# Kernel optimization log

Measured on AMD Instinct MI355X. Metric: run time of the kernel, lower is better.

The kernel has to match this reference:

```python
import jax, jax.numpy as jnp
import numpy as np

N_NEURONS = 100000
NNZ = 3200000
N_SENSORY = 5000
BATCH = 16
NUM_LAYERS = 8
THRESHOLD = 0.01
TANH_STEEPNESS = 5.0


def setup_inputs() -> dict:
    key = jax.random.key(0)
    k1, k2, k3, k4 = jax.random.split(key, 4)
    inputs = jax.random.uniform(k1, (BATCH, N_SENSORY, NUM_LAYERS), dtype=jnp.float32)
    # sparse connectome in COO form; small values so activations stay in a sane range
    weight_vals = jax.random.normal(k2, (NNZ,), dtype=jnp.float32) * 0.1
    weight_rows = jax.random.randint(k3, (NNZ,), 0, N_NEURONS, dtype=jnp.int32)
    weight_cols = jax.random.randint(k4, (NNZ,), 0, N_NEURONS, dtype=jnp.int32)
    sensory_indices = jnp.arange(N_SENSORY, dtype=jnp.int32)
    return {
        "inputs": inputs,
        "weight_vals": weight_vals,
        "weight_rows": weight_rows,
        "weight_cols": weight_cols,
        "sensory_indices": sensory_indices,
    }


def _spmm(vals, rows, cols, x):
    # x: (N, B); y[r, b] = sum_{e: rows[e]==r} vals[e] * x[cols[e], b]
    return jax.ops.segment_sum(vals[:, None] * x[cols], rows, num_segments=N_NEURONS)


def _activate(y):
    y = jnp.where(y >= THRESHOLD, y, jnp.zeros_like(y))
    return jnp.tanh(TANH_STEEPNESS * y)


def reference(inputs, weight_vals, weight_rows, weight_cols, sensory_indices):
    B, S, T = inputs.shape  # T == num_layers
    # preprocess sensory input: threshold then clamp to <= 1
    inp = jnp.where(inputs >= THRESHOLD, inputs, jnp.zeros_like(inputs))
    inp = jnp.minimum(inp, jnp.ones_like(inp))
    # state x: (N, B)
    full_input = jnp.zeros((N_NEURONS, B), inputs.dtype).at[sensory_indices].add(inp[:, :, 0].T)
    x = _activate(_spmm(weight_vals, weight_rows, weight_cols, full_input))
    acts = []
    for layer in range(1, T):
        # inject sensory input for this time step and clamp to <= 1
        x = x.at[sensory_indices].add(inp[:, :, layer].T)
        x = jnp.minimum(x, jnp.ones_like(x))
        acts.append(x)
        x = _activate(_spmm(weight_vals, weight_rows, weight_cols, x))
    acts.append(x)  # last layer: no injection
    # (T, N, B) -> (B, N, T), matching torch vmap'd cat along time dim
    return jnp.stack(acts, axis=0).transpose(2, 1, 0)
```

## Files before the change

kernel.cpp:

```cpp
#include <hip/hip_runtime.h>


#define N_NEURONS 100000
#define NNZ_CNT   3200000
#define N_SENSORY 5000
#define BATCH     16
#define T_LAYERS  8
#define THRESH    0.01f
#define STEEP     5.0f

#define NB (N_NEURONS * BATCH)
#define NT (N_NEURONS * T_LAYERS)
#define ST (N_SENSORY * T_LAYERS)

#define FXSCALE   17592186044416.0f
#define FXINV     (1.0 / 17592186044416.0)

#define LBITS   9
#define BROWS   (1 << LBITS)
#define NBUCKET ((N_NEURONS + BROWS - 1) / BROWS)
#define EPB     8192
#define NBLK_A  ((NNZ_CNT + EPB - 1) / EPB)

__device__ __forceinline__ float thresh_clamp_inp(float u) {
    u = (u >= THRESH) ? u : 0.0f;
    return fminf(u, 1.0f);
}
__device__ __forceinline__ float activate(float y) {
    y = (y >= THRESH) ? y : 0.0f;
    return tanhf(STEEP * y);
}


__global__ void k_init(const float* __restrict__ inp, float* __restrict__ state0,
                       int* __restrict__ btotal) {
    int stride = gridDim.x * blockDim.x;
    for (int i = blockIdx.x * blockDim.x + threadIdx.x; i < NB; i += stride) {
        int n = i >> 4, b = i & 15;
        float v = 0.0f;
        if (n < N_SENSORY) v = thresh_clamp_inp(inp[b * ST + n * T_LAYERS + 0]);
        state0[i] = v;
        if (i < NBUCKET) btotal[i] = 0;
    }
}

__global__ void __launch_bounds__(1024) k_bcount(const int* __restrict__ rows,
                                                 int* __restrict__ btotal) {
    __shared__ int cnt[NBUCKET];
    const int e0 = blockIdx.x * EPB;
    for (int i = threadIdx.x; i < NBUCKET; i += 1024) cnt[i] = 0;
    __syncthreads();
    #pragma unroll
    for (int i = 0; i < EPB / 1024; ++i) {
        int e = e0 + i * 1024 + threadIdx.x;
        if (e < NNZ_CNT) atomicAdd(&cnt[rows[e] >> LBITS], 1);
    }
    __syncthreads();
    for (int i = threadIdx.x; i < NBUCKET; i += 1024)
        if (cnt[i]) atomicAdd(&btotal[i], cnt[i]);
}

__global__ void k_bscan(const int* __restrict__ btotal, int* __restrict__ bbase,
                        int* __restrict__ bcur, int* __restrict__ row_ptr) {
    __shared__ int lds[256];
    int tid = threadIdx.x;
    int v = (tid < NBUCKET) ? btotal[tid] : 0;
    lds[tid] = v;
    __syncthreads();
    for (int off = 1; off < 256; off <<= 1) {
        int add = (tid >= off) ? lds[tid - off] : 0;
        __syncthreads();
        lds[tid] += add;
        __syncthreads();
    }
    if (tid < NBUCKET) {
        bbase[tid] = lds[tid] - v;
        bcur[tid]  = lds[tid] - v;
    }
    if (tid == 0) { bbase[NBUCKET] = NNZ_CNT; row_ptr[N_NEURONS] = NNZ_CNT; }
}

__global__ void __launch_bounds__(1024) k_passA(const float* __restrict__ vals,
                                                const int* __restrict__ rows,
                                                const int* __restrict__ cols,
                                                int* bcur,
                                                int2* __restrict__ packed_tmp) {
    __shared__ int cnt[NBUCKET];
    __shared__ int base[NBUCKET];
    const int e0 = blockIdx.x * EPB;
    for (int i = threadIdx.x; i < NBUCKET; i += 1024) cnt[i] = 0;
    __syncthreads();
    #pragma unroll
    for (int i = 0; i < EPB / 1024; ++i) {
        int e = e0 + i * 1024 + threadIdx.x;
        if (e < NNZ_CNT) atomicAdd(&cnt[rows[e] >> LBITS], 1);
    }
    __syncthreads();
    for (int i = threadIdx.x; i < NBUCKET; i += 1024) {
        int c = cnt[i];
        base[i] = (c > 0) ? atomicAdd(&bcur[i], c) : 0;
        cnt[i] = 0;
    }
    __syncthreads();
    #pragma unroll
    for (int i = 0; i < EPB / 1024; ++i) {
        int e = e0 + i * 1024 + threadIdx.x;
        if (e < NNZ_CNT) {
            int r = rows[e];
            int k = r >> LBITS;
            int pos = base[k] + atomicAdd(&cnt[k], 1);
            packed_tmp[pos] = make_int2((cols[e] << LBITS) | (r & (BROWS - 1)),
                                        __float_as_int(vals[e]));
        }
    }
}

__global__ void __launch_bounds__(1024) k_passB(const int* __restrict__ bbase,
                                                const int2* __restrict__ packed_tmp,
                                                int2* __restrict__ packed,
                                                int* __restrict__ row_ptr) {
    __shared__ int cnt[BROWS];
    __shared__ int scn[BROWS];
    const int tid = threadIdx.x;
    const int k  = blockIdx.x;
    const int r0 = k * BROWS;
    const int nr = min(BROWS, N_NEURONS - r0);
    const int P0 = bbase[k], P1 = bbase[k + 1];
    for (int i = tid; i < BROWS; i += 1024) cnt[i] = 0;
    __syncthreads();
    for (int i = P0 + tid; i < P1; i += 1024)
        atomicAdd(&cnt[packed_tmp[i].x & (BROWS - 1)], 1);
    __syncthreads();
    if (tid < BROWS) scn[tid] = cnt[tid];
    __syncthreads();
    for (int off = 1; off < BROWS; off <<= 1) {
        int add = (tid < BROWS && tid >= off) ? scn[tid - off] : 0;
        __syncthreads();
        if (tid < BROWS) scn[tid] += add;
        __syncthreads();
    }
    if (tid < BROWS) {
        int ex = P0 + scn[tid] - cnt[tid];
        if (tid < nr) row_ptr[r0 + tid] = ex;
        scn[tid] = ex;
    }
    __syncthreads();
    for (int i = P0 + tid; i < P1; i += 1024) {
        int2 pe = packed_tmp[i];
        int d = atomicAdd(&scn[pe.x & (BROWS - 1)], 1);
        packed[d] = make_int2(pe.x >> LBITS, pe.y);
    }
}

__global__ void __launch_bounds__(256) k_layer(const int* __restrict__ row_ptr,
                                               const int2* __restrict__ packed,
                                               const float* __restrict__ state_in,
                                               const float* __restrict__ inp,
                                               float* __restrict__ plane_out,
                                               int t) {
    int tid = blockIdx.x * blockDim.x + threadIdx.x;
    int r = tid >> 4, b = tid & 15;
    if (r >= N_NEURONS) return;
    int s = row_ptr[r], e = row_ptr[r + 1];
    long long acc = 0;
    for (int base = s; base < e; base += 16) {
        int idx = base + b;
        int2 pe = (idx < e) ? packed[idx] : make_int2(0, 0);
        #pragma unroll
        for (int j = 0; j < 16; ++j) {
            int   c = __shfl(pe.x, j, 16);
            float v = __int_as_float(__shfl(pe.y, j, 16));
            float xv = state_in[c * BATCH + b];
            acc += (long long)llrintf(v * xv * FXSCALE);
        }
    }
    float y = (float)((double)acc * FXINV);
    float a = activate(y);
    if (t < T_LAYERS - 1) {
        if (r < N_SENSORY) a += thresh_clamp_inp(inp[b * ST + r * T_LAYERS + (t + 1)]);
        a = fminf(a, 1.0f);
    }
    plane_out[r * BATCH + b] = a;
}

__global__ void k_out(const float* __restrict__ planes, float* __restrict__ out) {
    int i = blockIdx.x * blockDim.x + threadIdx.x;
    if (i >= NB) return;
    int n = i >> 4, b = i & 15;
    float4 o0, o1;
    o0.x = planes[0 * NB + i]; o0.y = planes[1 * NB + i];
    o0.z = planes[2 * NB + i]; o0.w = planes[3 * NB + i];
    o1.x = planes[4 * NB + i]; o1.y = planes[5 * NB + i];
    o1.z = planes[6 * NB + i]; o1.w = planes[7 * NB + i];
    float4* dst = (float4*)&out[b * NT + n * T_LAYERS];
    dst[0] = o0; dst[1] = o1;
}

__global__ void k2_init(const float* __restrict__ inp, float* __restrict__ state,
                        long long* __restrict__ acc) {
    int stride = gridDim.x * blockDim.x;
    for (int i = blockIdx.x * blockDim.x + threadIdx.x; i < NB; i += stride) {
        int n = i >> 4, b = i & 15;
        float v = 0.0f;
        if (n < N_SENSORY) v = thresh_clamp_inp(inp[b * ST + n * T_LAYERS + 0]);
        state[i] = v;
        acc[i]   = 0LL;
    }
}
__global__ void __launch_bounds__(256) k2_spmm(const float* __restrict__ vals,
                                               const int* __restrict__ rows,
                                               const int* __restrict__ cols,
                                               const float* __restrict__ state,
                                               long long* acc) {
    int tid = blockIdx.x * blockDim.x + threadIdx.x;
    int b = tid & 15;
    int e = tid >> 4;
    int estride = (gridDim.x * blockDim.x) >> 4;
    for (; e < NNZ_CNT; e += estride) {
        int   c  = cols[e];
        float xv = state[c * BATCH + b];
        float v  = vals[e];
        long long fx = llrintf(v * xv * FXSCALE);
        if (fx != 0LL) {
            int r = rows[e];
            atomicAdd((unsigned long long*)&acc[r * BATCH + b], (unsigned long long)fx);
        }
    }
}
__global__ void k2_act_inject(long long* acc, const float* __restrict__ inp,
                              float* __restrict__ state, float* __restrict__ out, int t) {
    int stride = gridDim.x * blockDim.x;
    for (int i = blockIdx.x * blockDim.x + threadIdx.x; i < NB; i += stride) {
        int n = i >> 4, b = i & 15;
        float y = (float)((double)acc[i] * FXINV);
        acc[i] = 0LL;
        float v = activate(y);
        if (n < N_SENSORY) v += thresh_clamp_inp(inp[b * ST + n * T_LAYERS + (t + 1)]);
        v = fminf(v, 1.0f);
        state[i] = v;
        out[b * NT + n * T_LAYERS + t] = v;
    }
}
__global__ void k2_act_final(const long long* __restrict__ acc, float* __restrict__ out) {
    int stride = gridDim.x * blockDim.x;
    for (int i = blockIdx.x * blockDim.x + threadIdx.x; i < NB; i += stride) {
        int n = i >> 4, b = i & 15;
        float y = (float)((double)acc[i] * FXINV);
        out[b * NT + n * T_LAYERS + (T_LAYERS - 1)] = activate(y);
    }
}

extern "C" void kernel_launch(void* const* d_in, const int* in_sizes, int n_in,
                              void* d_out, int out_size, void* d_ws, size_t ws_size,
                              hipStream_t stream) {
    const float* inputs = (const float*)d_in[0];
    const float* vals   = (const float*)d_in[1];
    const int*   rows   = (const int*)  d_in[2];
    const int*   cols   = (const int*)  d_in[3];
    float* out = (float*)d_out;

    const size_t sz_planes = (size_t)T_LAYERS * NB * 4;
    const size_t sz_packed = (size_t)NNZ_CNT * 8;
    const size_t sz_rowptr = ((size_t)N_NEURONS + 2) * 4;
    const size_t sz_btotal = (size_t)(NBUCKET + 8) * 4;
    const size_t sz_bbase  = (size_t)(NBUCKET + 8) * 4;
    const size_t sz_bcur   = (size_t)(NBUCKET + 8) * 4;
    const size_t REQ = sz_planes + sz_packed + sz_rowptr + sz_btotal + sz_bbase + sz_bcur;

    const int block = 256;

    if (ws_size >= REQ) {
        char* ws = (char*)d_ws;
        float* planes  = (float*)ws;
        int2*  packed  = (int2*)(ws + sz_planes);
        int*   row_ptr = (int*)(ws + sz_planes + sz_packed);
        int*   btotal  = (int*)(ws + sz_planes + sz_packed + sz_rowptr);
        int*   bbase   = (int*)(ws + sz_planes + sz_packed + sz_rowptr + sz_btotal);
        int*   bcur    = (int*)(ws + sz_planes + sz_packed + sz_rowptr + sz_btotal + sz_bbase);
        float* state0  = planes + (size_t)(T_LAYERS - 1) * NB;
        int2*  packed_tmp = (int2*)planes;

        const int grid_nb = (NB + block - 1) / block;

        k_init<<<grid_nb, block, 0, stream>>>(inputs, state0, btotal);
        k_bcount<<<NBLK_A, 1024, 0, stream>>>(rows, btotal);
        k_bscan<<<1, 256, 0, stream>>>(btotal, bbase, bcur, row_ptr);
        k_passA<<<NBLK_A, 1024, 0, stream>>>(vals, rows, cols, bcur, packed_tmp);
        k_passB<<<NBUCKET, 1024, 0, stream>>>(bbase, packed_tmp, packed, row_ptr);

        for (int t = 0; t < T_LAYERS; ++t) {
            const float* sin_ = (t == 0) ? state0 : planes + (size_t)(t - 1) * NB;
            k_layer<<<grid_nb, block, 0, stream>>>(row_ptr, packed, sin_, inputs,
                                                   planes + (size_t)t * NB, t);
        }
        k_out<<<grid_nb, block, 0, stream>>>(planes, out);
    } else {
        long long* acc   = (long long*)d_ws;
        float*     state = (float*)(acc + NB);
        const int grid_ew = 2048, grid_sp = 2048;
        k2_init<<<grid_ew, block, 0, stream>>>(inputs, state, acc);
        for (int t = 0; t < T_LAYERS; ++t) {
            k2_spmm<<<grid_sp, block, 0, stream>>>(vals, rows, cols, state, acc);
            if (t < T_LAYERS - 1)
                k2_act_inject<<<grid_ew, block, 0, stream>>>(acc, inputs, state, out, t);
            else
                k2_act_final<<<grid_ew, block, 0, stream>>>(acc, out);
        }
    }
}
```

Measured before the change: 426.6 us.

## Drop per-row CSR sort; accumulate bucketed edges in LDS with 64-bit atomics

Removes the second sorting pass (passB) and the row_ptr array. Edges are now grouped only into 128-row buckets. Each layer kernel block handles one bucket and accumulates fixed-point products into a shared-memory array with 64-bit LDS atomics, skipping products that are zero. This removes a full pass over the 3.2M edges and exposes more blocks, at the cost of LDS atomic contention and 16 KB of shared memory per block in every layer.

```diff
diff --git a/kernel.cpp b/kernel.cpp
--- a/kernel.cpp
+++ b/kernel.cpp
@@ -16,7 +16,7 @@
 #define FXSCALE   17592186044416.0f
 #define FXINV     (1.0 / 17592186044416.0)
 
-#define LBITS   9
+#define LBITS   7
 #define BROWS   (1 << LBITS)
 #define NBUCKET ((N_NEURONS + BROWS - 1) / BROWS)
 #define EPB     8192
@@ -34,14 +34,13 @@
 
 __global__ void k_init(const float* __restrict__ inp, float* __restrict__ state0,
                        int* __restrict__ btotal) {
-    int stride = gridDim.x * blockDim.x;
-    for (int i = blockIdx.x * blockDim.x + threadIdx.x; i < NB; i += stride) {
-        int n = i >> 4, b = i & 15;
-        float v = 0.0f;
-        if (n < N_SENSORY) v = thresh_clamp_inp(inp[b * ST + n * T_LAYERS + 0]);
-        state0[i] = v;
-        if (i < NBUCKET) btotal[i] = 0;
-    }
+    int i = blockIdx.x * blockDim.x + threadIdx.x;
+    if (i >= NB) return;
+    int n = i >> 4, b = i & 15;
+    float v = 0.0f;
+    if (n < N_SENSORY) v = thresh_clamp_inp(inp[b * ST + n * T_LAYERS + 0]);
+    state0[i] = v;
+    if (i < NBUCKET) btotal[i] = 0;
 }
 
 __global__ void __launch_bounds__(1024) k_bcount(const int* __restrict__ rows,
@@ -60,14 +59,15 @@
         if (cnt[i]) atomicAdd(&btotal[i], cnt[i]);
 }
 
-__global__ void k_bscan(const int* __restrict__ btotal, int* __restrict__ bbase,
-                        int* __restrict__ bcur, int* __restrict__ row_ptr) {
-    __shared__ int lds[256];
+__global__ void __launch_bounds__(1024) k_bscan(const int* __restrict__ btotal,
+                                                int* __restrict__ bbase,
+                                                int* __restrict__ bcur) {
+    __shared__ int lds[1024];
     int tid = threadIdx.x;
     int v = (tid < NBUCKET) ? btotal[tid] : 0;
     lds[tid] = v;
     __syncthreads();
-    for (int off = 1; off < 256; off <<= 1) {
+    for (int off = 1; off < 1024; off <<= 1) {
         int add = (tid >= off) ? lds[tid - off] : 0;
         __syncthreads();
         lds[tid] += add;
@@ -77,14 +77,14 @@
         bbase[tid] = lds[tid] - v;
         bcur[tid]  = lds[tid] - v;
     }
-    if (tid == 0) { bbase[NBUCKET] = NNZ_CNT; row_ptr[N_NEURONS] = NNZ_CNT; }
+    if (tid == 0) bbase[NBUCKET] = NNZ_CNT;
 }
 
 __global__ void __launch_bounds__(1024) k_passA(const float* __restrict__ vals,
                                                 const int* __restrict__ rows,
                                                 const int* __restrict__ cols,
                                                 int* bcur,
-                                                int2* __restrict__ packed_tmp) {
+                                                int2* __restrict__ slab) {
     __shared__ int cnt[NBUCKET];
     __shared__ int base[NBUCKET];
     const int e0 = blockIdx.x * EPB;
@@ -109,78 +109,55 @@
             int r = rows[e];
             int k = r >> LBITS;
             int pos = base[k] + atomicAdd(&cnt[k], 1);
-            packed_tmp[pos] = make_int2((cols[e] << LBITS) | (r & (BROWS - 1)),
-                                        __float_as_int(vals[e]));
-        }
-    }
-}
-
-__global__ void __launch_bounds__(1024) k_passB(const int* __restrict__ bbase,
-                                                const int2* __restrict__ packed_tmp,
-                                                int2* __restrict__ packed,
-                                                int* __restrict__ row_ptr) {
-    __shared__ int cnt[BROWS];
-    __shared__ int scn[BROWS];
-    const int tid = threadIdx.x;
-    const int k  = blockIdx.x;
-    const int r0 = k * BROWS;
-    const int nr = min(BROWS, N_NEURONS - r0);
-    const int P0 = bbase[k], P1 = bbase[k + 1];
-    for (int i = tid; i < BROWS; i += 1024) cnt[i] = 0;
-    __syncthreads();
-    for (int i = P0 + tid; i < P1; i += 1024)
-        atomicAdd(&cnt[packed_tmp[i].x & (BROWS - 1)], 1);
-    __syncthreads();
-    if (tid < BROWS) scn[tid] = cnt[tid];
-    __syncthreads();
-    for (int off = 1; off < BROWS; off <<= 1) {
-        int add = (tid < BROWS && tid >= off) ? scn[tid - off] : 0;
-        __syncthreads();
-        if (tid < BROWS) scn[tid] += add;
-        __syncthreads();
-    }
-    if (tid < BROWS) {
-        int ex = P0 + scn[tid] - cnt[tid];
-        if (tid < nr) row_ptr[r0 + tid] = ex;
-        scn[tid] = ex;
-    }
-    __syncthreads();
-    for (int i = P0 + tid; i < P1; i += 1024) {
-        int2 pe = packed_tmp[i];
-        int d = atomicAdd(&scn[pe.x & (BROWS - 1)], 1);
-        packed[d] = make_int2(pe.x >> LBITS, pe.y);
-    }
-}
-
-__global__ void __launch_bounds__(256) k_layer(const int* __restrict__ row_ptr,
-                                               const int2* __restrict__ packed,
+            slab[pos] = make_int2((cols[e] << LBITS) | (r & (BROWS - 1)),
+                                  __float_as_int(vals[e]));
+        }
+    }
+}
+
+__global__ void __launch_bounds__(256) k_layer(const int* __restrict__ bbase,
+                                               const int2* __restrict__ slab,
                                                const float* __restrict__ state_in,
                                                const float* __restrict__ inp,
                                                float* __restrict__ plane_out,
                                                int t) {
-    int tid = blockIdx.x * blockDim.x + threadIdx.x;
-    int r = tid >> 4, b = tid & 15;
-    if (r >= N_NEURONS) return;
-    int s = row_ptr[r], e = row_ptr[r + 1];
-    long long acc = 0;
-    for (int base = s; base < e; base += 16) {
+    __shared__ unsigned long long acc[BROWS * BATCH];
+    const int tid = threadIdx.x;
+    const int k = blockIdx.x;
+    const int r0 = k * BROWS;
+    for (int i = tid; i < BROWS * BATCH; i += 256) acc[i] = 0ull;
+    __syncthreads();
+    const int P0 = bbase[k], P1 = bbase[k + 1];
+    const int g = tid >> 4, b = tid & 15;
+    for (int base = P0 + g * 16; base < P1; base += 256) {
         int idx = base + b;
-        int2 pe = (idx < e) ? packed[idx] : make_int2(0, 0);
+        int2 pe = (idx < P1) ? slab[idx] : make_int2(0, 0);
         #pragma unroll
         for (int j = 0; j < 16; ++j) {
-            int   c = __shfl(pe.x, j, 16);
-            float v = __int_as_float(__shfl(pe.y, j, 16));
-            float xv = state_in[c * BATCH + b];
-            acc += (long long)llrintf(v * xv * FXSCALE);
-        }
-    }
-    float y = (float)((double)acc * FXINV);
-    float a = activate(y);
-    if (t < T_LAYERS - 1) {
-        if (r < N_SENSORY) a += thresh_clamp_inp(inp[b * ST + r * T_LAYERS + (t + 1)]);
-        a = fminf(a, 1.0f);
-    }
-    plane_out[r * BATCH + b] = a;
+            int   lo = __shfl(pe.x, j, 16);
+            float v  = __int_as_float(__shfl(pe.y, j, 16));
+            int   c  = lo >> LBITS;
+            int   lr = lo & (BROWS - 1);
+            float prod = v * state_in[c * BATCH + b];
+            if (prod != 0.0f) {
+                long long fx = llrintf(prod * FXSCALE);
+                atomicAdd(&acc[lr * BATCH + b], (unsigned long long)fx);
+            }
+        }
+    }
+    __syncthreads();
+    const int rend = min(BROWS, N_NEURONS - r0);
+    for (int i = tid; i < rend * BATCH; i += 256) {
+        int lr = i >> 4, bb = i & 15;
+        float y = (float)((double)(long long)acc[i] * FXINV);
+        float a = activate(y);
+        int r = r0 + lr;
+        if (t < T_LAYERS - 1) {
+            if (r < N_SENSORY) a += thresh_clamp_inp(inp[bb * ST + r * T_LAYERS + (t + 1)]);
+            a = fminf(a, 1.0f);
+        }
+        plane_out[r * BATCH + bb] = a;
+    }
 }
 
 __global__ void k_out(const float* __restrict__ planes, float* __restrict__ out) {
@@ -217,14 +194,10 @@
     int e = tid >> 4;
     int estride = (gridDim.x * blockDim.x) >> 4;
     for (; e < NNZ_CNT; e += estride) {
-        int   c  = cols[e];
-        float xv = state[c * BATCH + b];
-        float v  = vals[e];
-        long long fx = llrintf(v * xv * FXSCALE);
-        if (fx != 0LL) {
-            int r = rows[e];
-            atomicAdd((unsigned long long*)&acc[r * BATCH + b], (unsigned long long)fx);
-        }
+        float xv = state[cols[e] * BATCH + b];
+        long long fx = llrintf(vals[e] * xv * FXSCALE);
+        if (fx != 0LL)
+            atomicAdd((unsigned long long*)&acc[rows[e] * BATCH + b], (unsigned long long)fx);
     }
 }
 __global__ void k2_act_inject(long long* acc, const float* __restrict__ inp,
@@ -260,37 +233,31 @@
     float* out = (float*)d_out;
 
     const size_t sz_planes = (size_t)T_LAYERS * NB * 4;
-    const size_t sz_packed = (size_t)NNZ_CNT * 8;
-    const size_t sz_rowptr = ((size_t)N_NEURONS + 2) * 4;
-    const size_t sz_btotal = (size_t)(NBUCKET + 8) * 4;
-    const size_t sz_bbase  = (size_t)(NBUCKET + 8) * 4;
-    const size_t sz_bcur   = (size_t)(NBUCKET + 8) * 4;
-    const size_t REQ = sz_planes + sz_packed + sz_rowptr + sz_btotal + sz_bbase + sz_bcur;
+    const size_t sz_slab   = (size_t)NNZ_CNT * 8;
+    const size_t sz_bt     = (size_t)(NBUCKET + 8) * 4;
+    const size_t REQ = sz_planes + sz_slab + 3 * sz_bt;
 
     const int block = 256;
 
     if (ws_size >= REQ) {
         char* ws = (char*)d_ws;
-        float* planes  = (float*)ws;
-        int2*  packed  = (int2*)(ws + sz_planes);
-        int*   row_ptr = (int*)(ws + sz_planes + sz_packed);
-        int*   btotal  = (int*)(ws + sz_planes + sz_packed + sz_rowptr);
-        int*   bbase   = (int*)(ws + sz_planes + sz_packed + sz_rowptr + sz_btotal);
-        int*   bcur    = (int*)(ws + sz_planes + sz_packed + sz_rowptr + sz_btotal + sz_bbase);
-        float* state0  = planes + (size_t)(T_LAYERS - 1) * NB;
-        int2*  packed_tmp = (int2*)planes;
+        float* planes = (float*)ws;
+        int2*  slab   = (int2*)(ws + sz_planes);
+        int*   btotal = (int*)(ws + sz_planes + sz_slab);
+        int*   bbase  = (int*)(ws + sz_planes + sz_slab + sz_bt);
+        int*   bcur   = (int*)(ws + sz_planes + sz_slab + 2 * sz_bt);
+        float* state0 = planes + (size_t)(T_LAYERS - 1) * NB;
 
         const int grid_nb = (NB + block - 1) / block;
 
         k_init<<<grid_nb, block, 0, stream>>>(inputs, state0, btotal);
         k_bcount<<<NBLK_A, 1024, 0, stream>>>(rows, btotal);
-        k_bscan<<<1, 256, 0, stream>>>(btotal, bbase, bcur, row_ptr);
-        k_passA<<<NBLK_A, 1024, 0, stream>>>(vals, rows, cols, bcur, packed_tmp);
-        k_passB<<<NBUCKET, 1024, 0, stream>>>(bbase, packed_tmp, packed, row_ptr);
+        k_bscan<<<1, 1024, 0, stream>>>(btotal, bbase, bcur);
+        k_passA<<<NBLK_A, 1024, 0, stream>>>(vals, rows, cols, bcur, slab);
 
         for (int t = 0; t < T_LAYERS; ++t) {
             const float* sin_ = (t == 0) ? state0 : planes + (size_t)(t - 1) * NB;
-            k_layer<<<grid_nb, block, 0, stream>>>(row_ptr, packed, sin_, inputs,
+            k_layer<<<NBUCKET, block, 0, stream>>>(bbase, slab, sin_, inputs,
                                                    planes + (size_t)t * NB, t);
         }
         k_out<<<grid_nb, block, 0, stream>>>(planes, out);
```

After: 990.2 us. +132.1%, slower.

## Use 32-bit fixed-point accumulation with prescaled weights and LDS edge broadcast

Applied to the files above, without the earlier changes.

Weights are prescaled by 2^27 when packed, and the per-layer SpMM accumulates rounded products in 32-bit ints instead of 64-bit llrint at 2^44 scale. This removes the 64-bit conversions and adds, and it also replaces shuffle-based broadcast of edges with a shared-memory buffer. The bucketing pass block size is halved. The risks are lower precision and possible int overflow. The LDS buffer is written and read without a barrier, so correctness relies on 16-lane groups staying in lockstep within a wavefront.

```diff
diff --git a/kernel.cpp b/kernel.cpp
--- a/kernel.cpp
+++ b/kernel.cpp
@@ -13,14 +13,17 @@
 #define NT (N_NEURONS * T_LAYERS)
 #define ST (N_SENSORY * T_LAYERS)
 
-#define FXSCALE   17592186044416.0f
-#define FXINV     (1.0 / 17592186044416.0)
+#define FXS32     134217728.0f
+#define FXI32     7.450580596923828e-9f
 
 #define LBITS   9
 #define BROWS   (1 << LBITS)
 #define NBUCKET ((N_NEURONS + BROWS - 1) / BROWS)
-#define EPB     8192
+#define EPB     4096
 #define NBLK_A  ((NNZ_CNT + EPB - 1) / EPB)
+
+#define FXSCALE   17592186044416.0f
+#define FXINV     (1.0 / 17592186044416.0)
 
 __device__ __forceinline__ float thresh_clamp_inp(float u) {
     u = (u >= THRESH) ? u : 0.0f;
@@ -34,14 +37,13 @@
 
 __global__ void k_init(const float* __restrict__ inp, float* __restrict__ state0,
                        int* __restrict__ btotal) {
-    int stride = gridDim.x * blockDim.x;
-    for (int i = blockIdx.x * blockDim.x + threadIdx.x; i < NB; i += stride) {
-        int n = i >> 4, b = i & 15;
-        float v = 0.0f;
-        if (n < N_SENSORY) v = thresh_clamp_inp(inp[b * ST + n * T_LAYERS + 0]);
-        state0[i] = v;
-        if (i < NBUCKET) btotal[i] = 0;
-    }
+    int i = blockIdx.x * blockDim.x + threadIdx.x;
+    if (i >= NB) return;
+    int n = i >> 4, b = i & 15;
+    float v = 0.0f;
+    if (n < N_SENSORY) v = thresh_clamp_inp(inp[b * ST + n * T_LAYERS + 0]);
+    state0[i] = v;
+    if (i < NBUCKET) btotal[i] = 0;
 }
 
 __global__ void __launch_bounds__(1024) k_bcount(const int* __restrict__ rows,
@@ -84,7 +86,7 @@
                                                 const int* __restrict__ rows,
                                                 const int* __restrict__ cols,
                                                 int* bcur,
-                                                int2* __restrict__ packed_tmp) {
+                                                int2* __restrict__ slab) {
     __shared__ int cnt[NBUCKET];
     __shared__ int base[NBUCKET];
     const int e0 = blockIdx.x * EPB;
@@ -109,14 +111,14 @@
             int r = rows[e];
             int k = r >> LBITS;
             int pos = base[k] + atomicAdd(&cnt[k], 1);
-            packed_tmp[pos] = make_int2((cols[e] << LBITS) | (r & (BROWS - 1)),
-                                        __float_as_int(vals[e]));
+            slab[pos] = make_int2((cols[e] << LBITS) | (r & (BROWS - 1)),
+                                  __float_as_int(vals[e] * FXS32));
         }
     }
 }
 
 __global__ void __launch_bounds__(1024) k_passB(const int* __restrict__ bbase,
-                                                const int2* __restrict__ packed_tmp,
+                                                const int2* __restrict__ slab,
                                                 int2* __restrict__ packed,
                                                 int* __restrict__ row_ptr) {
     __shared__ int cnt[BROWS];
@@ -129,7 +131,7 @@
     for (int i = tid; i < BROWS; i += 1024) cnt[i] = 0;
     __syncthreads();
     for (int i = P0 + tid; i < P1; i += 1024)
-        atomicAdd(&cnt[packed_tmp[i].x & (BROWS - 1)], 1);
+        atomicAdd(&cnt[slab[i].x & (BROWS - 1)], 1);
     __syncthreads();
     if (tid < BROWS) scn[tid] = cnt[tid];
     __syncthreads();
@@ -146,7 +148,7 @@
     }
     __syncthreads();
     for (int i = P0 + tid; i < P1; i += 1024) {
-        int2 pe = packed_tmp[i];
+        int2 pe = slab[i];
         int d = atomicAdd(&scn[pe.x & (BROWS - 1)], 1);
         packed[d] = make_int2(pe.x >> LBITS, pe.y);
     }
@@ -158,23 +160,24 @@
                                                const float* __restrict__ inp,
                                                float* __restrict__ plane_out,
                                                int t) {
-    int tid = blockIdx.x * blockDim.x + threadIdx.x;
-    int r = tid >> 4, b = tid & 15;
-    if (r >= N_NEURONS) return;
-    int s = row_ptr[r], e = row_ptr[r + 1];
-    long long acc = 0;
+    __shared__ int2 ebuf[16][17];
+    const int tid = threadIdx.x;
+    const int g = tid >> 4, b = tid & 15;
+    const int r = blockIdx.x * 16 + g;
+    const int s = row_ptr[r], e = row_ptr[r + 1];
+    int acc = 0;
     for (int base = s; base < e; base += 16) {
         int idx = base + b;
         int2 pe = (idx < e) ? packed[idx] : make_int2(0, 0);
+        ebuf[g][b] = pe;
         #pragma unroll
         for (int j = 0; j < 16; ++j) {
-            int   c = __shfl(pe.x, j, 16);
-            float v = __int_as_float(__shfl(pe.y, j, 16));
-            float xv = state_in[c * BATCH + b];
-            acc += (long long)llrintf(v * xv * FXSCALE);
+            int2 q = ebuf[g][j];
+            float prod = __int_as_float(q.y) * state_in[q.x * BATCH + b];
+            acc += __float2int_rn(prod);
         }
     }
-    float y = (float)((double)acc * FXINV);
+    float y = (float)acc * FXI32;
     float a = activate(y);
     if (t < T_LAYERS - 1) {
         if (r < N_SENSORY) a += thresh_clamp_inp(inp[b * ST + r * T_LAYERS + (t + 1)]);
@@ -217,14 +220,10 @@
     int e = tid >> 4;
     int estride = (gridDim.x * blockDim.x) >> 4;
     for (; e < NNZ_CNT; e += estride) {
-        int   c  = cols[e];
-        float xv = state[c * BATCH + b];
-        float v  = vals[e];
-        long long fx = llrintf(v * xv * FXSCALE);
-        if (fx != 0LL) {
-            int r = rows[e];
-            atomicAdd((unsigned long long*)&acc[r * BATCH + b], (unsigned long long)fx);
-        }
+        float xv = state[cols[e] * BATCH + b];
+        long long fx = llrintf(vals[e] * xv * FXSCALE);
+        if (fx != 0LL)
+            atomicAdd((unsigned long long*)&acc[rows[e] * BATCH + b], (unsigned long long)fx);
     }
 }
 __global__ void k2_act_inject(long long* acc, const float* __restrict__ inp,
@@ -262,10 +261,8 @@
     const size_t sz_planes = (size_t)T_LAYERS * NB * 4;
     const size_t sz_packed = (size_t)NNZ_CNT * 8;
     const size_t sz_rowptr = ((size_t)N_NEURONS + 2) * 4;
-    const size_t sz_btotal = (size_t)(NBUCKET + 8) * 4;
-    const size_t sz_bbase  = (size_t)(NBUCKET + 8) * 4;
-    const size_t sz_bcur   = (size_t)(NBUCKET + 8) * 4;
-    const size_t REQ = sz_planes + sz_packed + sz_rowptr + sz_btotal + sz_bbase + sz_bcur;
+    const size_t sz_bt     = (size_t)(NBUCKET + 8) * 4;
+    const size_t REQ = sz_planes + sz_packed + sz_rowptr + 3 * sz_bt;
 
     const int block = 256;
 
@@ -275,18 +272,18 @@
         int2*  packed  = (int2*)(ws + sz_planes);
         int*   row_ptr = (int*)(ws + sz_planes + sz_packed);
         int*   btotal  = (int*)(ws + sz_planes + sz_packed + sz_rowptr);
-        int*   bbase   = (int*)(ws + sz_planes + sz_packed + sz_rowptr + sz_btotal);
-        int*   bcur    = (int*)(ws + sz_planes + sz_packed + sz_rowptr + sz_btotal + sz_bbase);
+        int*   bbase   = (int*)(ws + sz_planes + sz_packed + sz_rowptr + sz_bt);
+        int*   bcur    = (int*)(ws + sz_planes + sz_packed + sz_rowptr + 2 * sz_bt);
         float* state0  = planes + (size_t)(T_LAYERS - 1) * NB;
-        int2*  packed_tmp = (int2*)planes;
+        int2*  slab    = (int2*)planes;
 
         const int grid_nb = (NB + block - 1) / block;
 
         k_init<<<grid_nb, block, 0, stream>>>(inputs, state0, btotal);
         k_bcount<<<NBLK_A, 1024, 0, stream>>>(rows, btotal);
         k_bscan<<<1, 256, 0, stream>>>(btotal, bbase, bcur, row_ptr);
-        k_passA<<<NBLK_A, 1024, 0, stream>>>(vals, rows, cols, bcur, packed_tmp);
-        k_passB<<<NBUCKET, 1024, 0, stream>>>(bbase, packed_tmp, packed, row_ptr);
+        k_passA<<<NBLK_A, 1024, 0, stream>>>(vals, rows, cols, bcur, slab);
+        k_passB<<<NBUCKET, 1024, 0, stream>>>(bbase, slab, packed, row_ptr);
 
         for (int t = 0; t < T_LAYERS; ++t) {
             const float* sin_ = (t == 0) ? state0 : planes + (size_t)(t - 1) * NB;
```

Measured after the change: 400.8 us. 1.06x faster.
